# Optimization experiments

Hardware: AMD Instinct MI355X
Metric: run time of the kernel (lower is better)

## Reference

```python
import jax, jax.numpy as jnp
import numpy as np

B, T, F, D, H, L = 4, 1024, 128, 512, 8, 4
DFF = 4 * D
NE, MD = 16, 20
HD = D // H
SCALE = 1.0 / HD ** 0.5


def _ln(x, w, b):
    m = jnp.mean(x, axis=-1, keepdims=True)
    v = jnp.mean((x - m) ** 2, axis=-1, keepdims=True)
    return (x - m) * jax.lax.rsqrt(v + 1e-5) * w + b


def setup_inputs() -> dict:
    key = jax.random.key(0)
    ks = jax.random.split(key, 16)
    rn = lambda k, shape: jax.random.normal(k, shape, jnp.float32) * 0.02
    return {
        'node_features': jax.random.normal(ks[0], (B, T, F), jnp.float32),
        'centrality': jax.random.uniform(ks[1], (B, T), jnp.float32),
        'edge_types': jax.random.randint(ks[2], (B, T, T), 0, NE),
        'sp_dist': jax.random.randint(ks[3], (B, T, T), 0, MD + 1),
        'node_W': rn(ks[4], (F, D)), 'node_b': jnp.zeros((D,), jnp.float32),
        'cent_W': rn(ks[5], (D,)), 'cent_b': jnp.zeros((D,), jnp.float32),
        'edge_emb': rn(ks[6], (NE, H)), 'dist_emb': rn(ks[7], (MD + 1, H)),
        'ln1_w': jnp.ones((L, D), jnp.float32), 'ln1_b': jnp.zeros((L, D), jnp.float32),
        'q_W': rn(ks[8], (L, D, D)), 'q_b': jnp.zeros((L, D), jnp.float32),
        'k_W': rn(ks[9], (L, D, D)), 'k_b': jnp.zeros((L, D), jnp.float32),
        'v_W': rn(ks[10], (L, D, D)), 'v_b': jnp.zeros((L, D), jnp.float32),
        'o_W': rn(ks[11], (L, D, D)), 'o_b': jnp.zeros((L, D), jnp.float32),
        'ln2_w': jnp.ones((L, D), jnp.float32), 'ln2_b': jnp.zeros((L, D), jnp.float32),
        'f1_W': rn(ks[12], (L, D, DFF)), 'f1_b': jnp.zeros((L, DFF), jnp.float32),
        'f2_W': rn(ks[13], (L, DFF, D)), 'f2_b': jnp.zeros((L, D), jnp.float32),
    }


def _forward(node_features, centrality, edge_types, sp_dist,
             node_W, node_b, cent_W, cent_b, edge_emb, dist_emb,
             ln1_w, ln1_b, q_W, q_b, k_W, k_b, v_W, v_b, o_W, o_b,
             ln2_w, ln2_b, f1_W, f1_b, f2_W, f2_b):
    # node embedding + centrality encoding
    h = node_features @ node_W + node_b                      # [B,T,D]
    h = h + centrality[..., None] * cent_W + cent_b          # Linear(1,D)
    # Graphormer attention bias: [B,T,T,H] -> [B,H,T,T]
    sp = jnp.clip(sp_dist, 0, MD)
    attn_bias = (edge_emb[edge_types] + dist_emb[sp]).transpose(0, 3, 1, 2)

    def step(h, p):
        l1w, l1b, qW, qb, kW, kb, vW, vb, oW, ob, l2w, l2b, w1, b1, w2, b2 = p
        x = _ln(h, l1w, l1b)
        q = (x @ qW + qb).reshape(B, T, H, HD)
        k = (x @ kW + kb).reshape(B, T, H, HD)
        v = (x @ vW + vb).reshape(B, T, H, HD)
        scores = jnp.einsum('bihd,bjhd->bhij', q, k) * SCALE + attn_bias
        attn = jax.nn.softmax(scores, axis=-1)
        o = jnp.einsum('bhij,bjhd->bihd', attn, v).reshape(B, T, D)
        h = h + (o @ oW + ob)                                # dropout in eval mode
        x2 = _ln(h, l2w, l2b)
        h = h + (jax.nn.silu(x2 @ w1 + b1) @ w2 + b2)
        return h, None

    layer_params = (ln1_w, ln1_b, q_W, q_b, k_W, k_b, v_W, v_b, o_W, o_b,
                    ln2_w, ln2_b, f1_W, f1_b, f2_W, f2_b)
    h, _ = jax.lax.scan(step, h, layer_params)
    return h


def reference(node_features, centrality, edge_types, sp_dist,
              node_W, node_b, cent_W, cent_b, edge_emb, dist_emb,
              ln1_w, ln1_b, q_W, q_b, k_W, k_b, v_W, v_b, o_W, o_b,
              ln2_w, ln2_b, f1_W, f1_b, f2_W, f2_b):
    return _forward(node_features, centrality, edge_types, sp_dist,
                    node_W, node_b, cent_W, cent_b, edge_emb, dist_emb,
                    ln1_w, ln1_b, q_W, q_b, k_W, k_b, v_W, v_b, o_W, o_b,
                    ln2_w, ln2_b, f1_W, f1_b, f2_W, f2_b)
```

## Files before the change

kernel.cpp:

```cpp
#include <hip/hip_runtime.h>
#include <cstddef>
#include <cstdint>

#define B_    4
#define T_    1024
#define F_    128
#define D_    512
#define H_    8
#define L_    4
#define DFF_  2048
#define HD_   64
#define SCALE_ 0.125f
#define LOG2E_ 1.4426950408889634f
#define CL2E_  (SCALE_ * LOG2E_)

typedef __attribute__((ext_vector_type(8))) short bf16x8;
typedef __attribute__((ext_vector_type(4))) float f32x4;

#define AS1(p) ((const __attribute__((address_space(1))) void*)(p))
#define AS3(p) ((__attribute__((address_space(3))) void*)(p))

__device__ __forceinline__ short f2bf(float f) {
    unsigned u = __float_as_uint(f);
    u += 0x7FFFu + ((u >> 16) & 1u);
    return (short)(u >> 16);
}
__device__ __forceinline__ float bf2f(short s) {
    return __uint_as_float(((unsigned)(unsigned short)s) << 16);
}

#define PIPE_BARRIER(rem, W2, W1)                                             \
    if ((rem) >= 2)      asm volatile("s_waitcnt vmcnt(" #W2 ")" ::: "memory"); \
    else if ((rem) == 1) asm volatile("s_waitcnt vmcnt(" #W1 ")" ::: "memory"); \
    else                 asm volatile("s_waitcnt vmcnt(0)"      ::: "memory"); \
    __builtin_amdgcn_s_barrier();                                             \
    __builtin_amdgcn_sched_barrier(0);

__global__ __launch_bounds__(256) void ln_k(
    const float* __restrict__ X, const float* __restrict__ w,
    const float* __restrict__ b, short* __restrict__ Y)
{
    const int row = blockIdx.x;
    const int tid = threadIdx.x;
    const float* xr = X + (size_t)row * D_;
    const float v0 = xr[tid];
    const float v1 = xr[tid + 256];
    float s  = v0 + v1;
    float s2 = v0 * v0 + v1 * v1;
#pragma unroll
    for (int off = 1; off < 64; off <<= 1) {
        s  += __shfl_xor(s,  off);
        s2 += __shfl_xor(s2, off);
    }
    __shared__ float ss[4], ss2[4];
    if ((tid & 63) == 0) { ss[tid >> 6] = s; ss2[tid >> 6] = s2; }
    __syncthreads();
    s  = ss[0]  + ss[1]  + ss[2]  + ss[3];
    s2 = ss2[0] + ss2[1] + ss2[2] + ss2[3];
    const float mean = s * (1.f / D_);
    const float var  = s2 * (1.f / D_) - mean * mean;
    const float r    = rsqrtf(var + 1e-5f);
    short* yr = Y + (size_t)row * D_;
    yr[tid]       = f2bf((v0 - mean) * r * w[tid]       + b[tid]);
    yr[tid + 256] = f2bf((v1 - mean) * r * w[tid + 256] + b[tid + 256]);
}

__global__ __launch_bounds__(256) void transpose_all_k(
    const float* __restrict__ qW, const float* __restrict__ kW,
    const float* __restrict__ vW, const float* __restrict__ oW,
    const float* __restrict__ f1W, const float* __restrict__ f2W,
    const float* __restrict__ nW,
    short* __restrict__ WqkvT, short* __restrict__ WoT,
    short* __restrict__ Wf1T, short* __restrict__ Wf2T,
    short* __restrict__ nWt)
{
    const int id = blockIdx.y;
    const float* src; short* dst; int K, N;
    if (id < 12) {
        const int l = id / 3, which = id % 3;
        const float* s3 = (which == 0) ? qW : (which == 1) ? kW : vW;
        src = s3 + (size_t)l * D_ * D_;
        dst = WqkvT + ((size_t)l * 3 + which) * D_ * D_;
        K = D_; N = D_;
    } else if (id < 16) {
        const int l = id - 12;
        src = oW + (size_t)l * D_ * D_;  dst = WoT + (size_t)l * D_ * D_;
        K = D_; N = D_;
    } else if (id < 20) {
        const int l = id - 16;
        src = f1W + (size_t)l * D_ * DFF_;  dst = Wf1T + (size_t)l * DFF_ * D_;
        K = D_; N = DFF_;
    } else if (id < 24) {
        const int l = id - 20;
        src = f2W + (size_t)l * DFF_ * D_;  dst = Wf2T + (size_t)l * D_ * DFF_;
        K = DFF_; N = D_;
    } else {
        src = nW; dst = nWt; K = F_; N = D_;
    }
    const int ntiles = (K >> 5) * (N >> 5);
    if ((int)blockIdx.x >= ntiles) return;
    const int nt = N >> 5;
    const int k0 = (blockIdx.x / nt) << 5, n0 = (blockIdx.x % nt) << 5;

    __shared__ float t[32][33];
    const int c = threadIdx.x, r0 = threadIdx.y;
#pragma unroll
    for (int i = 0; i < 32; i += 8)
        t[r0 + i][c] = src[(size_t)(k0 + r0 + i) * N + n0 + c];
    __syncthreads();
#pragma unroll
    for (int i = 0; i < 32; i += 8)
        dst[(size_t)(n0 + r0 + i) * K + k0 + c] = f2bf(t[c][r0 + i]);
}

__global__ __launch_bounds__(256) void prep_k(
    const int* __restrict__ et, const int* __restrict__ sp,
    const float* __restrict__ ee, const float* __restrict__ de,
    unsigned char* __restrict__ biasT8,
    const float* __restrict__ nf, short* __restrict__ nfb,
    const float* __restrict__ qb, const float* __restrict__ kb,
    const float* __restrict__ vb, float* __restrict__ biasf)
{
    const int bid = blockIdx.x;
    const int tid = threadIdx.x;
    if (bid >= 4096) {
        if (bid < 4608) {
            const int i = (((bid - 4096) << 8) + tid) << 2;
            const float4 v = *(const float4*)(nf + i);
            *(short4*)(nfb + i) =
                make_short4(f2bf(v.x), f2bf(v.y), f2bf(v.z), f2bf(v.w));
        } else {
            const int i = ((bid - 4608) << 8) + tid;
            const int l = i / 1536, c = i % 1536;
            float v;
            if (c < 512)       v = qb[l * 512 + c];
            else if (c < 1024) v = kb[l * 512 + c - 512];
            else               v = vb[l * 512 + c - 1024];
            biasf[i] = v;
        }
        return;
    }
    __shared__ float eeS[16][8], deS[21][8];
    if (tid < 128) eeS[tid >> 3][tid & 7] = ee[tid];
    for (int t = tid; t < 168; t += 256)
        deS[t >> 3][t & 7] = de[t];
    __syncthreads();
    const int gid = bid * 256 + tid;
    const int j4  = (gid & 255) << 2;
    const int bi  = gid >> 8;
    const size_t base = (size_t)bi * T_ + j4;
    const int4 e = *(const int4*)(et + base);
    const int4 s = *(const int4*)(sp + base);
    const int b = bi >> 10, i = bi & 1023;
    const int ex[4] = {e.x, e.y, e.z, e.w};
    const int sx[4] = {min(s.x, 20), min(s.y, 20), min(s.z, 20), min(s.w, 20)};
#pragma unroll
    for (int h = 0; h < 8; ++h) {
        uchar4 o;
        float v;
        v = (eeS[ex[0]][h] + deS[sx[0]][h]) * LOG2E_ + 0.5f;
        o.x = (unsigned char)(int)fminf(fmaxf(v * 255.f + 0.5f, 0.f), 255.f);
        v = (eeS[ex[1]][h] + deS[sx[1]][h]) * LOG2E_ + 0.5f;
        o.y = (unsigned char)(int)fminf(fmaxf(v * 255.f + 0.5f, 0.f), 255.f);
        v = (eeS[ex[2]][h] + deS[sx[2]][h]) * LOG2E_ + 0.5f;
        o.z = (unsigned char)(int)fminf(fmaxf(v * 255.f + 0.5f, 0.f), 255.f);
        v = (eeS[ex[3]][h] + deS[sx[3]][h]) * LOG2E_ + 0.5f;
        o.w = (unsigned char)(int)fminf(fmaxf(v * 255.f + 0.5f, 0.f), 255.f);
        *(uchar4*)(biasT8 + ((size_t)((b * H_ + h) * T_ + i)) * T_ + j4) = o;
    }
}

__global__ __launch_bounds__(256) void embed_mm_k(
    const short* __restrict__ A, const short* __restrict__ Wt,
    const float* __restrict__ nb, const float* __restrict__ cb,
    const float* __restrict__ cW, const float* __restrict__ cent,
    float* __restrict__ C)
{
    const int K = F_, N = D_;
    __shared__ short As[4][128 * 32];
    __shared__ short Bs[4][64 * 32];
    const int tid  = threadIdx.x;
    const int lane = tid & 63, wv = tid >> 6;
    const int lb = blockIdx.x;
    const int xcd = lb & 7, jj = lb >> 3;
    const int bx = jj & 7, by = (xcd << 2) + (jj >> 3);
    const int bm = by << 7, bn = bx << 6;
    const int wm = (wv & 1) << 6, wn = (wv >> 1) << 5;

    const int c0 = (wv << 6) + lane;
    const int m0 = c0 >> 2, q0 = (c0 & 3) ^ ((m0 >> 1) & 3);
    const int c1 = 256 + c0;
    const int m1 = c1 >> 2, q1 = (c1 & 3) ^ ((m1 >> 1) & 3);

    const short* gA0 = A  + (size_t)(bm + m0) * K + (q0 << 3);
    const short* gA1 = A  + (size_t)(bm + m1) * K + (q1 << 3);
    const short* gB0 = Wt + (size_t)(bn + m0) * K + (q0 << 3);

    f32x4 acc[4][2];
#pragma unroll
    for (int i = 0; i < 4; ++i)
#pragma unroll
        for (int j = 0; j < 2; ++j)
            acc[i][j] = (f32x4){0.f, 0.f, 0.f, 0.f};

    const int fm = lane & 15, fq = lane >> 4;
    int caddr[4], baddr[2];
#pragma unroll
    for (int t = 0; t < 4; ++t) {
        const int rowA = wm + (t << 4) + fm;
        caddr[t] = ((rowA << 2) + (fq ^ ((rowA >> 1) & 3))) << 3;
    }
#pragma unroll
    for (int t = 0; t < 2; ++t) {
        const int rowB = wn + (t << 4) + fm;
        baddr[t] = ((rowB << 2) + (fq ^ ((rowB >> 1) & 3))) << 3;
    }

#define EMB_STAGE(KK, BUF) do { \
    __builtin_amdgcn_global_load_lds(AS1(gA0 + (KK)), AS3(&As[BUF][(wv << 9)]),        16, 0, 0); \
    __builtin_amdgcn_global_load_lds(AS1(gA1 + (KK)), AS3(&As[BUF][2048 + (wv << 9)]), 16, 0, 0); \
    __builtin_amdgcn_global_load_lds(AS1(gB0 + (KK)), AS3(&Bs[BUF][(wv << 9)]),        16, 0, 0); \
} while (0)

    EMB_STAGE(0, 0); EMB_STAGE(32, 1); EMB_STAGE(64, 2);
    const int nt = K >> 5;
    for (int t = 0; t < nt; ++t) {
        const int rem = nt - 1 - t;
        PIPE_BARRIER(rem, 6, 3);
        if (rem >= 3) EMB_STAGE((t + 3) << 5, (t + 3) & 3);
        const short* Asc = As[t & 3];
        const short* Bsc = Bs[t & 3];
        bf16x8 af[4], bf[2];
#pragma unroll
        for (int u = 0; u < 4; ++u) af[u] = *(const bf16x8*)(Asc + caddr[u]);
#pragma unroll
        for (int u = 0; u < 2; ++u) bf[u] = *(const bf16x8*)(Bsc + baddr[u]);
#pragma unroll
        for (int i = 0; i < 4; ++i)
#pragma unroll
            for (int j = 0; j < 2; ++j)
                acc[i][j] = __builtin_amdgcn_mfma_f32_16x16x32_bf16(
                    af[i], bf[j], acc[i][j], 0, 0, 0);
    }
#undef EMB_STAGE

    const int col0 = bn + wn + fm;
    const int row0 = bm + wm + (fq << 2);
#pragma unroll
    for (int j = 0; j < 2; ++j) {
        const int colg = col0 + (j << 4);
        const float bb = nb[colg] + cb[colg];
        const float cw = cW[colg];
#pragma unroll
        for (int i = 0; i < 4; ++i) {
#pragma unroll
            for (int r = 0; r < 4; ++r) {
                const int rowg = row0 + (i << 4) + r;
                C[(size_t)rowg * N + colg] = acc[i][j][r] + bb + cent[rowg] * cw;
            }
        }
    }
}

template <int OUTM, int ACT, int RES>
__global__ __launch_bounds__(256) void mm_k(
    const short* __restrict__ A, const short* __restrict__ Wt,
    const float* __restrict__ bias, const float* __restrict__ R,
    void* __restrict__ Cv, int M, int N, int K)
{
    __shared__ short As[4][128 * 32];
    __shared__ short Bs[4][128 * 32];
    const int tid  = threadIdx.x;
    const int lane = tid & 63, wv = tid >> 6;
    const int lb = blockIdx.x;
    const int xcd = lb & 7, jj = lb >> 3;
    const int bx = jj & 15, by = (xcd << 2) + (jj >> 4);
    const int bm = by << 7, bn = bx << 7;
    const int wm = (wv & 1) << 6, wn = (wv >> 1) << 6;

    const int c0 = (wv << 6) + lane;
    const int m0 = c0 >> 2, q0 = (c0 & 3) ^ ((m0 >> 1) & 3);
    const int c1 = 256 + c0;
    const int m1 = c1 >> 2, q1 = (c1 & 3) ^ ((m1 >> 1) & 3);

    const short* gA0 = A  + (size_t)(bm + m0) * K + (q0 << 3);
    const short* gA1 = A  + (size_t)(bm + m1) * K + (q1 << 3);
    const short* gB0 = Wt + (size_t)(bn + m0) * K + (q0 << 3);
    const short* gB1 = Wt + (size_t)(bn + m1) * K + (q1 << 3);

    f32x4 acc[4][4];
#pragma unroll
    for (int i = 0; i < 4; ++i)
#pragma unroll
        for (int j = 0; j < 4; ++j)
            acc[i][j] = (f32x4){0.f, 0.f, 0.f, 0.f};

    const int fm = lane & 15, fq = lane >> 4;
    int caddr[4], baddr[4];
#pragma unroll
    for (int t = 0; t < 4; ++t) {
        const int rowA = wm + (t << 4) + fm;
        caddr[t] = ((rowA << 2) + (fq ^ ((rowA >> 1) & 3))) << 3;
        const int rowB = wn + (t << 4) + fm;
        baddr[t] = ((rowB << 2) + (fq ^ ((rowB >> 1) & 3))) << 3;
    }

#define MM_STAGE(KK, BUF) do { \
    __builtin_amdgcn_global_load_lds(AS1(gA0 + (KK)), AS3(&As[BUF][(wv << 9)]),        16, 0, 0); \
    __builtin_amdgcn_global_load_lds(AS1(gA1 + (KK)), AS3(&As[BUF][2048 + (wv << 9)]), 16, 0, 0); \
    __builtin_amdgcn_global_load_lds(AS1(gB0 + (KK)), AS3(&Bs[BUF][(wv << 9)]),        16, 0, 0); \
    __builtin_amdgcn_global_load_lds(AS1(gB1 + (KK)), AS3(&Bs[BUF][2048 + (wv << 9)]), 16, 0, 0); \
} while (0)

    MM_STAGE(0, 0); MM_STAGE(32, 1); MM_STAGE(64, 2);
    const int nt = K >> 5;
    for (int t = 0; t < nt; ++t) {
        const int rem = nt - 1 - t;
        PIPE_BARRIER(rem, 8, 4);
        if (rem >= 3) MM_STAGE((t + 3) << 5, (t + 3) & 3);
        const short* Asc = As[t & 3];
        const short* Bsc = Bs[t & 3];
        bf16x8 af[4], bf[4];
#pragma unroll
        for (int u = 0; u < 4; ++u) {
            af[u] = *(const bf16x8*)(Asc + caddr[u]);
            bf[u] = *(const bf16x8*)(Bsc + baddr[u]);
        }
#pragma unroll
        for (int i = 0; i < 4; ++i)
#pragma unroll
            for (int j = 0; j < 4; ++j)
                acc[i][j] = __builtin_amdgcn_mfma_f32_16x16x32_bf16(
                    af[i], bf[j], acc[i][j], 0, 0, 0);
    }
#undef MM_STAGE

    const int col0 = bn + wn + fm;
    const int row0 = bm + wm + (fq << 2);
    float* Cf = (float*)Cv;
    short* Cb = (short*)Cv;
#pragma unroll
    for (int j = 0; j < 4; ++j) {
        const int colg = col0 + (j << 4);
        const float bb = bias[colg];
#pragma unroll
        for (int i = 0; i < 4; ++i) {
#pragma unroll
            for (int r = 0; r < 4; ++r) {
                const int rowg = row0 + (i << 4) + r;
                float v = acc[i][j][r] + bb;
                if (ACT) v = v / (1.f + __expf(-v));
                const size_t off = (size_t)rowg * N + colg;
                if (RES) v += R[off];
                if (OUTM == 1) Cb[off] = f2bf(v);
                else           Cf[off] = v;
            }
        }
    }
}

__global__ __launch_bounds__(256) void qkv64_k(
    const short* __restrict__ A, const short* __restrict__ Wt,
    const float* __restrict__ bias, short* __restrict__ QKb,
    short* __restrict__ VtOut)
{
    const int K = D_;
    __shared__ short As[4][128 * 32];
    __shared__ short Bs[4][64 * 32];
    const int tid  = threadIdx.x;
    const int lane = tid & 63, wv = tid >> 6;
    const int lb = blockIdx.x;
    const int xcd = lb & 7, jj = lb >> 3;
    const int yl = jj / 24, bx = jj - yl * 24;
    const int by = (xcd << 2) + yl;
    const int bm = by << 7, bn = bx << 6;
    const int wm = (wv & 1) << 6, wn = (wv >> 1) << 5;

    const int c0 = (wv << 6) + lane;
    const int m0 = c0 >> 2, q0 = (c0 & 3) ^ ((m0 >> 1) & 3);
    const int c1 = 256 + c0;
    const int m1 = c1 >> 2, q1 = (c1 & 3) ^ ((m1 >> 1) & 3);

    const short* gA0 = A  + (size_t)(bm + m0) * K + (q0 << 3);
    const short* gA1 = A  + (size_t)(bm + m1) * K + (q1 << 3);
    const short* gB0 = Wt + (size_t)(bn + m0) * K + (q0 << 3);

    f32x4 acc[4][2];
#pragma unroll
    for (int i = 0; i < 4; ++i)
#pragma unroll
        for (int j = 0; j < 2; ++j)
            acc[i][j] = (f32x4){0.f, 0.f, 0.f, 0.f};

    const int fm = lane & 15, fq = lane >> 4;
    int caddr[4], baddr[2];
#pragma unroll
    for (int t = 0; t < 4; ++t) {
        const int rowA = wm + (t << 4) + fm;
        caddr[t] = ((rowA << 2) + (fq ^ ((rowA >> 1) & 3))) << 3;
    }
#pragma unroll
    for (int t = 0; t < 2; ++t) {
        const int rowB = wn + (t << 4) + fm;
        baddr[t] = ((rowB << 2) + (fq ^ ((rowB >> 1) & 3))) << 3;
    }

#define QKV_STAGE(KK, BUF) do { \
    __builtin_amdgcn_global_load_lds(AS1(gA0 + (KK)), AS3(&As[BUF][(wv << 9)]),        16, 0, 0); \
    __builtin_amdgcn_global_load_lds(AS1(gA1 + (KK)), AS3(&As[BUF][2048 + (wv << 9)]), 16, 0, 0); \
    __builtin_amdgcn_global_load_lds(AS1(gB0 + (KK)), AS3(&Bs[BUF][(wv << 9)]),        16, 0, 0); \
} while (0)

    QKV_STAGE(0, 0); QKV_STAGE(32, 1); QKV_STAGE(64, 2);
    const int nt = K >> 5;
    for (int t = 0; t < nt; ++t) {
        const int rem = nt - 1 - t;
        PIPE_BARRIER(rem, 6, 3);
        if (rem >= 3) QKV_STAGE((t + 3) << 5, (t + 3) & 3);
        const short* Asc = As[t & 3];
        const short* Bsc = Bs[t & 3];
        bf16x8 af[4], bf[2];
#pragma unroll
        for (int u = 0; u < 4; ++u) af[u] = *(const bf16x8*)(Asc + caddr[u]);
#pragma unroll
        for (int u = 0; u < 2; ++u) bf[u] = *(const bf16x8*)(Bsc + baddr[u]);
#pragma unroll
        for (int i = 0; i < 4; ++i)
#pragma unroll
            for (int j = 0; j < 2; ++j)
                acc[i][j] = __builtin_amdgcn_mfma_f32_16x16x32_bf16(
                    af[i], bf[j], acc[i][j], 0, 0, 0);
    }
#undef QKV_STAGE

    const int col0 = bn + wn + fm;
    const int row0 = bm + wm + (fq << 2);
#pragma unroll
    for (int j = 0; j < 2; ++j) {
        const int colg = col0 + (j << 4);
        const float bb = bias[colg];
#pragma unroll
        for (int i = 0; i < 4; ++i) {
#pragma unroll
            for (int r = 0; r < 4; ++r) {
                const int rowg = row0 + (i << 4) + r;
                const float v = acc[i][j][r] + bb;
                if (colg < 1024) {
                    QKb[(size_t)rowg * 1024 + colg] = f2bf(v);
                } else {
                    const int da = colg - 1024;
                    const int hh = da >> 6, dd = da & 63;
                    const int bb2 = rowg >> 10, tt = rowg & 1023;
                    VtOut[((size_t)(bb2 * H_ + hh) * 64 + dd) * T_ + tt] = f2bf(v);
                }
            }
        }
    }
}

__global__ __launch_bounds__(256) void flash_k(
    const short* __restrict__ QKb, const short* __restrict__ Vt,
    const unsigned char* __restrict__ biasT8, short* __restrict__ OpartB,
    float* __restrict__ Lpart)
{
    const int tid = threadIdx.x;
    const int bx = blockIdx.x;
    const int it = bx >> 1, split = bx & 1;
    const int i0 = it << 6;
    const int h  = blockIdx.y;
    const int b  = blockIdx.z;
    const int lane = tid & 63, w = tid >> 6;
    const int fm = lane & 15, q = lane >> 4;

    __shared__ short Ks[4096];
    __shared__ short Vs[4096];
    __shared__ unsigned char Bsh8[4096];
    __shared__ short Ps[64][72];

    const short* qp = QKb + (size_t)(b * T_ + i0 + (w << 4) + fm) * 1024 + (h << 6) + (q << 3);
    const bf16x8 aq0 = *(const bf16x8*)(qp);
    const bf16x8 aq1 = *(const bf16x8*)(qp + 32);

    const int s0 = (w << 6) + lane, r0 = s0 >> 3, cc0 = (s0 & 7) ^ (r0 & 7);
    const int s1 = 256 + s0,        r1 = s1 >> 3, cc1 = (s1 & 7) ^ (r1 & 7);
    const short* gK0 = QKb + (size_t)(b * T_ + r0) * 1024 + 512 + (h << 6) + (cc0 << 3);
    const short* gK1 = QKb + (size_t)(b * T_ + r1) * 1024 + 512 + (h << 6) + (cc1 << 3);
    const short* gV0 = Vt + ((size_t)((b * H_ + h) << 6) + r0) * T_ + (cc0 << 3);
    const short* gV1 = Vt + ((size_t)((b * H_ + h) << 6) + r1) * T_ + (cc1 << 3);
    const int br = s0 >> 2, bc = (s0 & 3) ^ (br & 3);
    const unsigned char* gB0 = biasT8 +
        ((size_t)(b * H_ + h) * T_ + i0 + br) * T_ + (bc << 4);

    int fAddr[4][2];
#pragma unroll
    for (int t = 0; t < 4; ++t) {
        const int row = (t << 4) + fm;
#pragma unroll
        for (int ks = 0; ks < 2; ++ks)
            fAddr[t][ks] = (row << 6) + (((q + (ks << 2)) ^ (row & 7)) << 3);
    }

    int bAddr[4][4];
#pragma unroll
    for (int r = 0; r < 4; ++r) {
        const int rowL = (w << 4) + (q << 2) + r;
#pragma unroll
        for (int jt = 0; jt < 4; ++jt)
            bAddr[r][jt] = (rowL << 6) + (((jt ^ (rowL & 3))) << 4) + fm;
    }

    const short oneb = 0x3F80;
    const bf16x8 ones = {oneb, oneb, oneb, oneb, oneb, oneb, oneb, oneb};

    f32x4 accO[4];
#pragma unroll
    for (int dt = 0; dt < 4; ++dt) accO[dt] = (f32x4){0.f, 0.f, 0.f, 0.f};
    f32x4 accL = (f32x4){0.f, 0.f, 0.f, 0.f};

    const int irow = b * T_ + i0 + (w << 4) + (q << 2);
    short* psW = &Ps[(w << 4) + (q << 2)][fm];
    const short* psR = &Ps[(w << 4) + fm][q << 3];

    const int jbeg = split << 9, jend = jbeg + 512;
    for (int j0 = jbeg; j0 < jend; j0 += 64) {
        __syncthreads();
        __builtin_amdgcn_global_load_lds(AS1(gK0 + (size_t)j0 * 1024), AS3(Ks + (s0 << 3)), 16, 0, 0);
        __builtin_amdgcn_global_load_lds(AS1(gK1 + (size_t)j0 * 1024), AS3(Ks + (s1 << 3)), 16, 0, 0);
        __builtin_amdgcn_global_load_lds(AS1(gV0 + j0), AS3(Vs + (s0 << 3)), 16, 0, 0);
        __builtin_amdgcn_global_load_lds(AS1(gV1 + j0), AS3(Vs + (s1 << 3)), 16, 0, 0);
        __builtin_amdgcn_global_load_lds(AS1(gB0 + j0), AS3(Bsh8 + (s0 << 4)), 16, 0, 0);
        __syncthreads();

        f32x4 s[4];
#pragma unroll
        for (int jt = 0; jt < 4; ++jt) s[jt] = (f32x4){0.f, 0.f, 0.f, 0.f};
#pragma unroll
        for (int jt = 0; jt < 4; ++jt) {
            const bf16x8 k0 = *(const bf16x8*)(Ks + fAddr[jt][0]);
            const bf16x8 k1 = *(const bf16x8*)(Ks + fAddr[jt][1]);
            s[jt] = __builtin_amdgcn_mfma_f32_16x16x32_bf16(aq0, k0, s[jt], 0, 0, 0);
            s[jt] = __builtin_amdgcn_mfma_f32_16x16x32_bf16(aq1, k1, s[jt], 0, 0, 0);
        }

#pragma unroll
        for (int r = 0; r < 4; ++r)
#pragma unroll
            for (int jt = 0; jt < 4; ++jt) {
                const float q8 = (float)Bsh8[bAddr[r][jt]];
                const float bb = fmaf(q8, 1.f / 255.f, -0.5f);
                const float p = __builtin_amdgcn_exp2f(fmaf(s[jt][r], CL2E_, bb));
                psW[(size_t)r * 72 + (jt << 4)] = f2bf(p);
            }

#pragma unroll
        for (int ks = 0; ks < 2; ++ks) {
            const bf16x8 ap = *(const bf16x8*)(psR + (ks << 5));
            accL = __builtin_amdgcn_mfma_f32_16x16x32_bf16(ap, ones, accL, 0, 0, 0);
#pragma unroll
            for (int dt = 0; dt < 4; ++dt) {
                const bf16x8 bv = *(const bf16x8*)(Vs + fAddr[dt][ks]);
                accO[dt] = __builtin_amdgcn_mfma_f32_16x16x32_bf16(ap, bv, accO[dt], 0, 0, 0);
            }
        }
    }

    short* obase = OpartB + (size_t)split * B_ * T_ * D_;
#pragma unroll
    for (int r = 0; r < 4; ++r) {
        short* op = obase + (size_t)(irow + r) * D_ + (h << 6) + fm;
#pragma unroll
        for (int dt = 0; dt < 4; ++dt)
            op[dt << 4] = f2bf(accO[dt][r]);
    }
    if (fm == 0) {
#pragma unroll
        for (int r = 0; r < 4; ++r)
            Lpart[(size_t)split * B_ * T_ * H_ + (size_t)(irow + r) * H_ + h] = accL[r];
    }
}

__global__ __launch_bounds__(256) void combine_k(
    const short* __restrict__ OpartB, const float* __restrict__ Lpart,
    short* __restrict__ Ob)
{
    const int gid = blockIdx.x * 256 + threadIdx.x;
    const int d4  = (gid & 127) << 2;
    const int row = gid >> 7;
    const int h   = d4 >> 6;
    const float l = Lpart[(size_t)row * H_ + h] +
                    Lpart[(size_t)B_ * T_ * H_ + (size_t)row * H_ + h];
    const float inv = 1.f / l;
    const size_t o = (size_t)row * D_ + d4;
    const short4 a = *(const short4*)(OpartB + o);
    const short4 c = *(const short4*)(OpartB + (size_t)B_ * T_ * D_ + o);
    short4 r = make_short4(
        f2bf((bf2f(a.x) + bf2f(c.x)) * inv), f2bf((bf2f(a.y) + bf2f(c.y)) * inv),
        f2bf((bf2f(a.z) + bf2f(c.z)) * inv), f2bf((bf2f(a.w) + bf2f(c.w)) * inv));
    *(short4*)(Ob + o) = r;
}

__global__ __launch_bounds__(256) void mm64_k(
    const short* __restrict__ A, const short* __restrict__ Wt,
    const float* __restrict__ bias, const float* __restrict__ R,
    float* __restrict__ C, int M, int N, int K)
{
    __shared__ short As[4][128 * 32];
    __shared__ short Bs[4][64 * 32];
    const int tid  = threadIdx.x;
    const int lane = tid & 63, wv = tid >> 6;
    const int lb = blockIdx.x;
    const int xcd = lb & 7, jj = lb >> 3;
    const int bx = jj & 7, by = (xcd << 2) + (jj >> 3);
    const int bm = by << 7, bn = bx << 6;
    const int wm = (wv & 1) << 6, wn = (wv >> 1) << 5;

    const int c0 = (wv << 6) + lane;
    const int m0 = c0 >> 2, q0 = (c0 & 3) ^ ((m0 >> 1) & 3);
    const int c1 = 256 + c0;
    const int m1 = c1 >> 2, q1 = (c1 & 3) ^ ((m1 >> 1) & 3);

    const short* gA0 = A  + (size_t)(bm + m0) * K + (q0 << 3);
    const short* gA1 = A  + (size_t)(bm + m1) * K + (q1 << 3);
    const short* gB0 = Wt + (size_t)(bn + m0) * K + (q0 << 3);

    f32x4 acc[4][2];
#pragma unroll
    for (int i = 0; i < 4; ++i)
#pragma unroll
        for (int j = 0; j < 2; ++j)
            acc[i][j] = (f32x4){0.f, 0.f, 0.f, 0.f};

    const int fm = lane & 15, fq = lane >> 4;
    int caddr[4], baddr[2];
#pragma unroll
    for (int t = 0; t < 4; ++t) {
        const int rowA = wm + (t << 4) + fm;
        caddr[t] = ((rowA << 2) + (fq ^ ((rowA >> 1) & 3))) << 3;
    }
#pragma unroll
    for (int t = 0; t < 2; ++t) {
        const int rowB = wn + (t << 4) + fm;
        baddr[t] = ((rowB << 2) + (fq ^ ((rowB >> 1) & 3))) << 3;
    }

#define MM64_STAGE(KK, BUF) do { \
    __builtin_amdgcn_global_load_lds(AS1(gA0 + (KK)), AS3(&As[BUF][(wv << 9)]),        16, 0, 0); \
    __builtin_amdgcn_global_load_lds(AS1(gA1 + (KK)), AS3(&As[BUF][2048 + (wv << 9)]), 16, 0, 0); \
    __builtin_amdgcn_global_load_lds(AS1(gB0 + (KK)), AS3(&Bs[BUF][(wv << 9)]),        16, 0, 0); \
} while (0)

    MM64_STAGE(0, 0); MM64_STAGE(32, 1); MM64_STAGE(64, 2);
    const int nt = K >> 5;
    for (int t = 0; t < nt; ++t) {
        const int rem = nt - 1 - t;
        PIPE_BARRIER(rem, 6, 3);
        if (rem >= 3) MM64_STAGE((t + 3) << 5, (t + 3) & 3);
        const short* Asc = As[t & 3];
        const short* Bsc = Bs[t & 3];
        bf16x8 af[4], bf[2];
#pragma unroll
        for (int u = 0; u < 4; ++u) af[u] = *(const bf16x8*)(Asc + caddr[u]);
#pragma unroll
        for (int u = 0; u < 2; ++u) bf[u] = *(const bf16x8*)(Bsc + baddr[u]);
#pragma unroll
        for (int i = 0; i < 4; ++i)
#pragma unroll
            for (int j = 0; j < 2; ++j)
                acc[i][j] = __builtin_amdgcn_mfma_f32_16x16x32_bf16(
                    af[i], bf[j], acc[i][j], 0, 0, 0);
    }
#undef MM64_STAGE

    const int col0 = bn + wn + fm;
    const int row0 = bm + wm + (fq << 2);
#pragma unroll
    for (int j = 0; j < 2; ++j) {
        const int colg = col0 + (j << 4);
        const float bb = bias[colg];
#pragma unroll
        for (int i = 0; i < 4; ++i) {
#pragma unroll
            for (int r = 0; r < 4; ++r) {
                const int rowg = row0 + (i << 4) + r;
                const size_t off = (size_t)rowg * N + colg;
                C[off] = acc[i][j][r] + bb + R[off];
            }
        }
    }
}

extern "C" void kernel_launch(void* const* d_in, const int* in_sizes, int n_in,
                              void* d_out, int out_size, void* d_ws, size_t ws_size,
                              hipStream_t stream)
{
    (void)in_sizes; (void)n_in; (void)out_size; (void)ws_size;

    const float* nf   = (const float*)d_in[0];
    const float* cent = (const float*)d_in[1];
    const int*   et   = (const int*)  d_in[2];
    const int*   sp   = (const int*)  d_in[3];
    const float* nW   = (const float*)d_in[4];
    const float* nb   = (const float*)d_in[5];
    const float* cW   = (const float*)d_in[6];
    const float* cb   = (const float*)d_in[7];
    const float* ee   = (const float*)d_in[8];
    const float* de   = (const float*)d_in[9];
    const float* ln1w = (const float*)d_in[10];
    const float* ln1b = (const float*)d_in[11];
    const float* qW   = (const float*)d_in[12];
    const float* qb   = (const float*)d_in[13];
    const float* kW   = (const float*)d_in[14];
    const float* kb   = (const float*)d_in[15];
    const float* vW   = (const float*)d_in[16];
    const float* vb   = (const float*)d_in[17];
    const float* oW   = (const float*)d_in[18];
    const float* ob   = (const float*)d_in[19];
    const float* ln2w = (const float*)d_in[20];
    const float* ln2b = (const float*)d_in[21];
    const float* f1W  = (const float*)d_in[22];
    const float* f1b  = (const float*)d_in[23];
    const float* f2W  = (const float*)d_in[24];
    const float* f2b  = (const float*)d_in[25];

    const int M = B_ * T_;
    char* p = (char*)d_ws;
    float* Hbuf  = (float*)p;  p += (size_t)M * D_ * 4;
    short* QKb   = (short*)p;  p += (size_t)M * 1024 * 2;
    short* Vt    = (short*)p;  p += (size_t)B_ * H_ * 64 * T_ * 2;
    float* biasf = (float*)p;  p += (size_t)L_ * 3 * D_ * 4;
    short* Xbuf  = (short*)p;  p += (size_t)M * D_ * 2;
    short* Ob    = (short*)p;  p += (size_t)M * D_ * 2;
    short* FF    = (short*)p;  p += (size_t)M * DFF_ * 2;
    unsigned char* biasT8 = (unsigned char*)p; p += (size_t)B_ * H_ * T_ * T_;
    short* WqkvT = (short*)p;  p += (size_t)L_ * 3 * D_ * D_ * 2;
    short* WoT   = (short*)p;  p += (size_t)L_ * D_ * D_ * 2;
    short* Wf1T  = (short*)p;  p += (size_t)L_ * DFF_ * D_ * 2;
    short* Wf2T  = (short*)p;  p += (size_t)L_ * D_ * DFF_ * 2;
    short* nfb   = (short*)p;  p += (size_t)M * F_ * 2;
    short* nWt   = (short*)p;  p += (size_t)D_ * F_ * 2;
    short* OpartB = (short*)p; p += (size_t)2 * M * D_ * 2;
    float* Lpart = (float*)p;  p += (size_t)2 * M * H_ * 4;

    float* out = (float*)d_out;

    transpose_all_k<<<dim3(1024, 25), dim3(32, 8), 0, stream>>>(
        qW, kW, vW, oW, f1W, f2W, nW, WqkvT, WoT, Wf1T, Wf2T, nWt);
    prep_k<<<dim3(4632), dim3(256), 0, stream>>>(
        et, sp, ee, de, biasT8, nf, nfb, qb, kb, vb, biasf);
    embed_mm_k<<<dim3(256), dim3(256), 0, stream>>>(
        nfb, nWt, nb, cb, cW, cent, Hbuf);

    const dim3 blk(256);
    const dim3 gQKV(768);
    const dim3 gO64(256);
    const dim3 gF1 (512);
    const dim3 gAttn(2 * T_ / 64, H_, B_);
    const dim3 gCmb(M * D_ / 1024);

    for (int l = 0; l < L_; ++l) {
        const size_t bOff  = (size_t)l * D_;
        const size_t b1Off = (size_t)l * DFF_;

        ln_k<<<dim3(M), blk, 0, stream>>>(Hbuf, ln1w + bOff, ln1b + bOff, Xbuf);

        qkv64_k<<<gQKV, blk, 0, stream>>>(
            Xbuf, WqkvT + (size_t)l * 3 * D_ * D_, biasf + (size_t)l * 3 * D_,
            QKb, Vt);

        flash_k<<<gAttn, blk, 0, stream>>>(QKb, Vt, biasT8, OpartB, Lpart);
        combine_k<<<gCmb, blk, 0, stream>>>(OpartB, Lpart, Ob);

        mm64_k<<<gO64, blk, 0, stream>>>(
            Ob, WoT + (size_t)l * D_ * D_, ob + bOff, Hbuf, Hbuf, M, D_, D_);

        ln_k<<<dim3(M), blk, 0, stream>>>(Hbuf, ln2w + bOff, ln2b + bOff, Xbuf);

        mm_k<1, 1, 0><<<gF1, blk, 0, stream>>>(
            Xbuf, Wf1T + (size_t)l * DFF_ * D_, f1b + b1Off, nullptr, FF, M, DFF_, D_);

        float* cdst = (l == L_ - 1) ? out : Hbuf;
        mm64_k<<<gO64, blk, 0, stream>>>(
            FF, Wf2T + (size_t)l * D_ * DFF_, f2b + bOff, Hbuf, cdst, M, D_, DFF_);
    }
}
```

Measured before the change: 655.8 us.

## Split-K the O-proj and FF2 GEMMs and fuse partial reduction into layernorm

The O-projection and FF2 GEMMs now split K in two, doubling the grid from 256 to 512 blocks, and write two fp32 partial outputs instead of adding the residual in the epilogue. The following layernorm kernel sums the residual with both partials, writes the updated hidden state back, and normalizes. A final reduction kernel produces the output. This aims to fill more CUs on the small-grid GEMMs, at the cost of extra fp32 partial traffic and another kernel launch.

```diff
diff --git a/kernel.cpp b/kernel.cpp
--- a/kernel.cpp
+++ b/kernel.cpp
@@ -36,15 +36,25 @@
     __builtin_amdgcn_s_barrier();                                             \
     __builtin_amdgcn_sched_barrier(0);
 
+template <int NP>
 __global__ __launch_bounds__(256) void ln_k(
-    const float* __restrict__ X, const float* __restrict__ w,
+    float* __restrict__ X, const float* __restrict__ P0,
+    const float* __restrict__ P1, const float* __restrict__ w,
     const float* __restrict__ b, short* __restrict__ Y)
 {
     const int row = blockIdx.x;
     const int tid = threadIdx.x;
-    const float* xr = X + (size_t)row * D_;
-    const float v0 = xr[tid];
-    const float v1 = xr[tid + 256];
+    float* xr = X + (size_t)row * D_;
+    float v0 = xr[tid];
+    float v1 = xr[tid + 256];
+    if (NP == 2) {
+        const size_t o0 = (size_t)row * D_ + tid;
+        const size_t o1 = o0 + 256;
+        v0 += P0[o0] + P1[o0];
+        v1 += P0[o1] + P1[o1];
+        xr[tid]       = v0;
+        xr[tid + 256] = v1;
+    }
     float s  = v0 + v1;
     float s2 = v0 * v0 + v1 * v1;
 #pragma unroll
@@ -63,6 +73,18 @@
     short* yr = Y + (size_t)row * D_;
     yr[tid]       = f2bf((v0 - mean) * r * w[tid]       + b[tid]);
     yr[tid + 256] = f2bf((v1 - mean) * r * w[tid + 256] + b[tid + 256]);
+}
+
+__global__ __launch_bounds__(256) void red_k(
+    const float* __restrict__ X, const float* __restrict__ P0,
+    const float* __restrict__ P1, float* __restrict__ Dst)
+{
+    const int i = (blockIdx.x * 256 + threadIdx.x) << 2;
+    const float4 a = *(const float4*)(X + i);
+    const float4 p = *(const float4*)(P0 + i);
+    const float4 q = *(const float4*)(P1 + i);
+    *(float4*)(Dst + i) = make_float4(a.x + p.x + q.x, a.y + p.y + q.y,
+                                      a.z + p.z + q.z, a.w + p.w + q.w);
 }
 
 __global__ __launch_bounds__(256) void transpose_all_k(
@@ -599,10 +621,10 @@
     *(short4*)(Ob + o) = r;
 }
 
-__global__ __launch_bounds__(256) void mm64_k(
+__global__ __launch_bounds__(256) void mm64p_k(
     const short* __restrict__ A, const short* __restrict__ Wt,
-    const float* __restrict__ bias, const float* __restrict__ R,
-    float* __restrict__ C, int M, int N, int K)
+    const float* __restrict__ bias, float* __restrict__ P,
+    int M, int N, int K, int KS)
 {
     __shared__ short As[4][128 * 32];
     __shared__ short Bs[4][64 * 32];
@@ -610,8 +632,11 @@
     const int lane = tid & 63, wv = tid >> 6;
     const int lb = blockIdx.x;
     const int xcd = lb & 7, jj = lb >> 3;
-    const int bx = jj & 7, by = (xcd << 2) + (jj >> 3);
+    const int z  = jj >> 5;
+    const int jr = jj & 31;
+    const int bx = jr & 7, by = (xcd << 2) + (jr >> 3);
     const int bm = by << 7, bn = bx << 6;
+    const int ks0 = z * KS;
     const int wm = (wv & 1) << 6, wn = (wv >> 1) << 5;
 
     const int c0 = (wv << 6) + lane;
@@ -619,9 +644,9 @@
     const int c1 = 256 + c0;
     const int m1 = c1 >> 2, q1 = (c1 & 3) ^ ((m1 >> 1) & 3);
 
-    const short* gA0 = A  + (size_t)(bm + m0) * K + (q0 << 3);
-    const short* gA1 = A  + (size_t)(bm + m1) * K + (q1 << 3);
-    const short* gB0 = Wt + (size_t)(bn + m0) * K + (q0 << 3);
+    const short* gA0 = A  + (size_t)(bm + m0) * K + ks0 + (q0 << 3);
+    const short* gA1 = A  + (size_t)(bm + m1) * K + ks0 + (q1 << 3);
+    const short* gB0 = Wt + (size_t)(bn + m0) * K + ks0 + (q0 << 3);
 
     f32x4 acc[4][2];
 #pragma unroll
@@ -650,7 +675,7 @@
 } while (0)
 
     MM64_STAGE(0, 0); MM64_STAGE(32, 1); MM64_STAGE(64, 2);
-    const int nt = K >> 5;
+    const int nt = KS >> 5;
     for (int t = 0; t < nt; ++t) {
         const int rem = nt - 1 - t;
         PIPE_BARRIER(rem, 6, 3);
@@ -673,17 +698,17 @@
 
     const int col0 = bn + wn + fm;
     const int row0 = bm + wm + (fq << 2);
+    float* Pz = P + (size_t)z * M * N;
 #pragma unroll
     for (int j = 0; j < 2; ++j) {
         const int colg = col0 + (j << 4);
-        const float bb = bias[colg];
+        const float bb = (z == 0) ? bias[colg] : 0.f;
 #pragma unroll
         for (int i = 0; i < 4; ++i) {
 #pragma unroll
             for (int r = 0; r < 4; ++r) {
                 const int rowg = row0 + (i << 4) + r;
-                const size_t off = (size_t)rowg * N + colg;
-                C[off] = acc[i][j][r] + bb + R[off];
+                Pz[(size_t)rowg * N + colg] = acc[i][j][r] + bb;
             }
         }
     }
@@ -740,6 +765,7 @@
     short* nWt   = (short*)p;  p += (size_t)D_ * F_ * 2;
     short* OpartB = (short*)p; p += (size_t)2 * M * D_ * 2;
     float* Lpart = (float*)p;  p += (size_t)2 * M * H_ * 4;
+    float* Pbuf  = (float*)p;  p += (size_t)2 * M * D_ * 4;
 
     float* out = (float*)d_out;
 
@@ -752,7 +778,7 @@
 
     const dim3 blk(256);
     const dim3 gQKV(768);
-    const dim3 gO64(256);
+    const dim3 gO64p(512);
     const dim3 gF1 (512);
     const dim3 gAttn(2 * T_ / 64, H_, B_);
     const dim3 gCmb(M * D_ / 1024);
@@ -761,7 +787,12 @@
         const size_t bOff  = (size_t)l * D_;
         const size_t b1Off = (size_t)l * DFF_;
 
-        ln_k<<<dim3(M), blk, 0, stream>>>(Hbuf, ln1w + bOff, ln1b + bOff, Xbuf);
+        if (l == 0)
+            ln_k<0><<<dim3(M), blk, 0, stream>>>(
+                Hbuf, nullptr, nullptr, ln1w + bOff, ln1b + bOff, Xbuf);
+        else
+            ln_k<2><<<dim3(M), blk, 0, stream>>>(
+                Hbuf, Pbuf, Pbuf + (size_t)M * D_, ln1w + bOff, ln1b + bOff, Xbuf);
 
         qkv64_k<<<gQKV, blk, 0, stream>>>(
             Xbuf, WqkvT + (size_t)l * 3 * D_ * D_, biasf + (size_t)l * 3 * D_,
@@ -770,16 +801,18 @@
         flash_k<<<gAttn, blk, 0, stream>>>(QKb, Vt, biasT8, OpartB, Lpart);
         combine_k<<<gCmb, blk, 0, stream>>>(OpartB, Lpart, Ob);
 
-        mm64_k<<<gO64, blk, 0, stream>>>(
-            Ob, WoT + (size_t)l * D_ * D_, ob + bOff, Hbuf, Hbuf, M, D_, D_);
-
-        ln_k<<<dim3(M), blk, 0, stream>>>(Hbuf, ln2w + bOff, ln2b + bOff, Xbuf);
+        mm64p_k<<<gO64p, blk, 0, stream>>>(
+            Ob, WoT + (size_t)l * D_ * D_, ob + bOff, Pbuf, M, D_, D_, D_ / 2);
+
+        ln_k<2><<<dim3(M), blk, 0, stream>>>(
+            Hbuf, Pbuf, Pbuf + (size_t)M * D_, ln2w + bOff, ln2b + bOff, Xbuf);
 
         mm_k<1, 1, 0><<<gF1, blk, 0, stream>>>(
             Xbuf, Wf1T + (size_t)l * DFF_ * D_, f1b + b1Off, nullptr, FF, M, DFF_, D_);
 
-        float* cdst = (l == L_ - 1) ? out : Hbuf;
-        mm64_k<<<gO64, blk, 0, stream>>>(
-            FF, Wf2T + (size_t)l * D_ * DFF_, f2b + bOff, Hbuf, cdst, M, D_, DFF_);
-    }
-}
+        mm64p_k<<<gO64p, blk, 0, stream>>>(
+            FF, Wf2T + (size_t)l * D_ * DFF_, f2b + bOff, Pbuf, M, D_, DFF_, DFF_ / 2);
+    }
+
+    red_k<<<gCmb, blk, 0, stream>>>(Hbuf, Pbuf, Pbuf + (size_t)M * D_, out);
+}
```

New measurement: 623.4 us. 4.9% less time.
